# Kernel optimization log

Measured on AMD Instinct MI355X. Metric: run time of the kernel, lower is better.

Reference implementation:

```python
import jax, jax.numpy as jnp
import numpy as np

T_DIFF = 1000.0
LN_EPS = 1e-5


def _lin(x, w, b):
    return jnp.matmul(x, w.T) + b


def _ln(x, g, b):
    m = jnp.mean(x, axis=-1, keepdims=True)
    v = jnp.mean((x - m) ** 2, axis=-1, keepdims=True)
    return (x - m) / jnp.sqrt(v + LN_EPS) * g + b


def _pos_lin(x, w, b):
    return jnp.matmul(x, jax.nn.softplus(w).T) + b


def _gamma(t, g_l1_w, g_l1_b, g_l2_w, g_l2_b, g_l3_w, g_l3_b, gamma_0, gamma_1):
    def gtilde(u):
        l1 = _pos_lin(u, g_l1_w, g_l1_b)
        return l1 + _pos_lin(jax.nn.sigmoid(_pos_lin(l1, g_l2_w, g_l2_b)), g_l3_w, g_l3_b)
    g0, g1, gt = gtilde(jnp.zeros_like(t)), gtilde(jnp.ones_like(t)), gtilde(t)
    return gamma_0 + (gamma_1 - gamma_0) * (gt - g0) / (g1 - g0)


def _pair_dist(a):
    # safe pairwise euclidean distances, (B,N,N,1)
    diff = a[:, :, None, :] - a[:, None, :, :]
    d2 = jnp.sum(diff * diff, axis=-1, keepdims=True)
    return diff, jnp.sqrt(jnp.maximum(d2, 1e-12)), d2


def _egc_layer(x, h, x0, p):
    _, d0, _ = _pair_dist(x0)                      # original distances
    diff, dist, d2 = _pair_dist(x)                 # current distances (pre-LN x)
    h = _ln(h, p['lnh_g'], p['lnh_b'])
    x = _ln(x, p['lnx_g'], p['lnx_b'])
    B, N, F = h.shape
    h_i = jnp.broadcast_to(h[:, :, None, :], (B, N, N, F))
    h_j = jnp.broadcast_to(h[:, None, :, :], (B, N, N, F))
    einp = jnp.concatenate([h_i, h_j, d2, d0], axis=-1)  # (B,N,N,2F+2)
    m = jax.nn.silu(_lin(einp, p['edg1_w'], p['edg1_b']))
    m = jax.nn.silu(_lin(m, p['edg2_w'], p['edg2_b']))
    e = jax.nn.sigmoid(_lin(m, p['edgi_w'], p['edgi_b']))
    e = e * (1.0 - jnp.eye(N, dtype=e.dtype)[None, :, :, None])
    m_agg = jnp.sum(e * m, axis=2)                 # sum over j -> (B,N,F)
    hn = jax.nn.silu(_lin(jnp.concatenate([h, m_agg], axis=-1), p['node1_w'], p['node1_b']))
    hn = h + _lin(hn, p['node2_w'], p['node2_b'])
    cw = jax.nn.silu(_lin(einp, p['cor1_w'], p['cor1_b']))
    cw = jax.nn.silu(_lin(cw, p['cor2_w'], p['cor2_b']))
    cw = _lin(cw, p['cor3_w'], p['cor3_b'])        # (B,N,N,1)
    x_next = x + jnp.sum(cw * (diff / (dist + 1.0)), axis=2)
    return x_next, hn


def setup_inputs() -> dict:
    key = jax.random.key(0)
    ks = iter(jax.random.split(key, 64))
    B, N, H, L = 8, 192, 32, 4
    d = {}
    d['xyz_atom_species'] = jax.random.normal(next(ks), (B, N, 4), jnp.float32)
    d['pdf'] = jax.random.normal(next(ks), (B, 3000), jnp.float32)
    d['t'] = jax.random.uniform(next(ks), (B,), jnp.float32) * T_DIFF

    def w(k, shape):
        fan_in = shape[-1]
        return jax.random.normal(k, shape, jnp.float32) / np.sqrt(fan_in)

    d['emb_in_w'] = w(next(ks), (H, 12)); d['emb_in_b'] = jnp.zeros((H,), jnp.float32)
    d['emb_out_w'] = w(next(ks), (1, H)); d['emb_out_b'] = jnp.zeros((1,), jnp.float32)
    d['x_out_w'] = w(next(ks), (3, 3)); d['x_out_b'] = jnp.zeros((3,), jnp.float32)
    d['pdf_w'] = w(next(ks), (10, 3000)); d['pdf_b'] = jnp.zeros((10,), jnp.float32)
    d['g_l1_w'] = w(next(ks), (1, 1)); d['g_l1_b'] = jnp.zeros((1,), jnp.float32)
    d['g_l2_w'] = w(next(ks), (1024, 1)); d['g_l2_b'] = jnp.zeros((1024,), jnp.float32)
    d['g_l3_w'] = w(next(ks), (1, 1024)); d['g_l3_b'] = jnp.zeros((1,), jnp.float32)
    d['gamma_0'] = jnp.array([-5.0], jnp.float32)
    d['gamma_1'] = jnp.array([10.0], jnp.float32)
    d['lnh_g'] = jnp.ones((L, H), jnp.float32); d['lnh_b'] = jnp.zeros((L, H), jnp.float32)
    d['lnx_g'] = jnp.ones((L, 3), jnp.float32); d['lnx_b'] = jnp.zeros((L, 3), jnp.float32)
    d['edg1_w'] = w(next(ks), (L, H, 2 * H + 2)); d['edg1_b'] = jnp.zeros((L, H), jnp.float32)
    d['edg2_w'] = w(next(ks), (L, H, H)); d['edg2_b'] = jnp.zeros((L, H), jnp.float32)
    d['edgi_w'] = w(next(ks), (L, 1, H)); d['edgi_b'] = jnp.zeros((L, 1), jnp.float32)
    d['node1_w'] = w(next(ks), (L, H, 2 * H)); d['node1_b'] = jnp.zeros((L, H), jnp.float32)
    d['node2_w'] = w(next(ks), (L, H, H)); d['node2_b'] = jnp.zeros((L, H), jnp.float32)
    d['cor1_w'] = w(next(ks), (L, H, 2 * H + 2)); d['cor1_b'] = jnp.zeros((L, H), jnp.float32)
    d['cor2_w'] = w(next(ks), (L, H, H)); d['cor2_b'] = jnp.zeros((L, H), jnp.float32)
    d['cor3_w'] = w(next(ks), (L, 1, H)); d['cor3_b'] = jnp.zeros((L, 1), jnp.float32)
    return d


def reference(xyz_atom_species, pdf, t, emb_in_w, emb_in_b, emb_out_w, emb_out_b,
              x_out_w, x_out_b, pdf_w, pdf_b, g_l1_w, g_l1_b, g_l2_w, g_l2_b,
              g_l3_w, g_l3_b, gamma_0, gamma_1, lnh_g, lnh_b, lnx_g, lnx_b,
              edg1_w, edg1_b, edg2_w, edg2_b, edgi_w, edgi_b, node1_w, node1_b,
              node2_w, node2_b, cor1_w, cor1_b, cor2_w, cor2_b, cor3_w, cor3_b):
    B, N, _ = xyz_atom_species.shape
    h = xyz_atom_species[:, :, 3:4]                # (B,N,1)
    x = xyz_atom_species[:, :, :3]
    x0 = x
    tn = (t / T_DIFF)[:, None]                     # (B,1)
    t_emb = _gamma(tn, g_l1_w, g_l1_b, g_l2_w, g_l2_b, g_l3_w, g_l3_b, gamma_0, gamma_1)
    pdf_emb = _lin(pdf, pdf_w, pdf_b)              # (B,10)
    h = jnp.concatenate([
        h,
        jnp.broadcast_to(t_emb[:, None, :], (B, N, 1)),
        jnp.broadcast_to(pdf_emb[:, None, :], (B, N, 10)),
    ], axis=-1)
    h = _lin(h, emb_in_w, emb_in_b)                # (B,N,32)
    for l in range(4):
        p = dict(lnh_g=lnh_g[l], lnh_b=lnh_b[l], lnx_g=lnx_g[l], lnx_b=lnx_b[l],
                 edg1_w=edg1_w[l], edg1_b=edg1_b[l], edg2_w=edg2_w[l], edg2_b=edg2_b[l],
                 edgi_w=edgi_w[l], edgi_b=edgi_b[l], node1_w=node1_w[l], node1_b=node1_b[l],
                 node2_w=node2_w[l], node2_b=node2_b[l], cor1_w=cor1_w[l], cor1_b=cor1_b[l],
                 cor2_w=cor2_w[l], cor2_b=cor2_b[l], cor3_w=cor3_w[l], cor3_b=cor3_b[l])
        x, h = _egc_layer(x, h, x0, p)
    h = _lin(h, emb_out_w, emb_out_b)
    x = _lin(x, x_out_w, x_out_b) - x0
    return jnp.concatenate([x, h], axis=-1)        # (B,N,4)
```

## Files before the change

kernel.cpp:

```cpp
#include <hip/hip_runtime.h>
#include <hip/hip_bf16.h>
#include <math.h>

#define BATCH 8
#define NATOMS 192
#define HF 32

using short8 = __attribute__((ext_vector_type(8))) short;
using f32x4  = __attribute__((ext_vector_type(4))) float;

__device__ __forceinline__ float fast_rcp(float x){ return __builtin_amdgcn_rcpf(x); }
__device__ __forceinline__ float sigmoid_f(float x){ return fast_rcp(1.0f+__expf(-x)); }
__device__ __forceinline__ float silu_f(float x){ return x*fast_rcp(1.0f+__expf(-x)); }
__device__ __forceinline__ float softplus_f(float x){ return fmaxf(x,0.0f)+log1pf(expf(-fabsf(x))); }
__device__ __forceinline__ unsigned short f2bf(float x){
  __hip_bfloat16 h = __float2bfloat16(x);
  return __builtin_bit_cast(unsigned short, h);
}

__device__ __forceinline__ float wave_sum(float v){
  v += __shfl_xor(v, 1);
  v += __shfl_xor(v, 2);
  v += __shfl_xor(v, 4);
  v += __shfl_xor(v, 8);
  v += __shfl_xor(v, 16);
  v += __shfl_xor(v, 32);
  return v;
}

__global__ __launch_bounds__(256) void k_prelude(
    const float* __restrict__ pdf, const float* __restrict__ t,
    const float* __restrict__ pdf_w, const float* __restrict__ pdf_b,
    const float* __restrict__ g1w, const float* __restrict__ g1b,
    const float* __restrict__ g2w, const float* __restrict__ g2b,
    const float* __restrict__ g3w, const float* __restrict__ g3b,
    const float* __restrict__ gamma0, const float* __restrict__ gamma1,
    const float* __restrict__ e2w, const float* __restrict__ c2w,
    unsigned short* __restrict__ e2wb, unsigned short* __restrict__ c2wb,
    float* __restrict__ temb, float* __restrict__ pdfe)
{
  __shared__ float lds[4];
  const int bx = blockIdx.x, tid = threadIdx.x;
  const int wv = tid >> 6, ln = tid & 63;

  if (bx >= 88){
    const int g = (bx - 88)*256 + tid;
    e2wb[g] = f2bf(e2w[g]);
    c2wb[g] = f2bf(c2w[g]);
    return;
  }
  if (bx < 80){
    const int b = bx / 10, o = bx % 10;
    const float* pb = pdf + b*3000;
    const float* wb = pdf_w + o*3000;
    float p = 0.f;
    for (int k = tid; k < 3000; k += 256) p = fmaf(pb[k], wb[k], p);
    p = wave_sum(p);
    if (ln == 0) lds[wv] = p;
    __syncthreads();
    if (tid == 0) pdfe[b*10 + o] = lds[0] + lds[1] + lds[2] + lds[3] + pdf_b[o];
    return;
  }
  const int b = bx - 80;
  const float w1 = softplus_f(g1w[0]);
  const float b1 = g1b[0];
  const float tn = t[b] * (1.0f/1000.0f);
  const float l1_0 = b1;
  const float l1_1 = w1 + b1;
  const float l1_t = fmaf(w1, tn, b1);
  float a0 = 0.f, a1 = 0.f, at = 0.f;
  for (int k = tid; k < 1024; k += 256){
    float w2 = softplus_f(g2w[k]);
    float bb = g2b[k];
    float w3 = softplus_f(g3w[k]);
    a0 += sigmoid_f(fmaf(w2, l1_0, bb)) * w3;
    a1 += sigmoid_f(fmaf(w2, l1_1, bb)) * w3;
    at += sigmoid_f(fmaf(w2, l1_t, bb)) * w3;
  }
  float sums[3]; float vals[3] = {a0, a1, at};
  for (int r = 0; r < 3; ++r){
    float v = wave_sum(vals[r]);
    __syncthreads();
    if (ln == 0) lds[wv] = v;
    __syncthreads();
    sums[r] = lds[0] + lds[1] + lds[2] + lds[3];
  }
  if (tid == 0){
    const float b3 = g3b[0];
    const float g0 = l1_0 + sums[0] + b3;
    const float g1v = l1_1 + sums[1] + b3;
    const float gt = l1_t + sums[2] + b3;
    temb[b] = gamma0[0] + (gamma1[0] - gamma0[0]) * (gt - g0) / (g1v - g0);
  }
}

__global__ __launch_bounds__(256) void k_embed_node(
    const float* __restrict__ xyz, const float* __restrict__ temb,
    const float* __restrict__ pdfe, const float* __restrict__ wi,
    const float* __restrict__ bi,
    const float* __restrict__ lnhg, const float* __restrict__ lnhb,
    const float* __restrict__ e1w, const float* __restrict__ e1b,
    const float* __restrict__ c1w, const float* __restrict__ c1b,
    float* __restrict__ x, float* __restrict__ hln,
    float* __restrict__ ue, float* __restrict__ uc,
    float* __restrict__ vep, float* __restrict__ vcp)
{
  __shared__ float s_h[8][33];
  const int tid = threadIdx.x;
  const int il = tid >> 5, f = tid & 31;
  const int node = blockIdx.x*8 + il;
  const int b = node / NATOMS;

  {
    const float sp = xyz[node*4 + 3];
    const float* w = wi + f*12;
    float a = bi[f];
    a = fmaf(sp, w[0], a);
    a = fmaf(temb[b], w[1], a);
    const float* pe = pdfe + b*10;
#pragma unroll
    for (int p = 0; p < 10; ++p) a = fmaf(pe[p], w[2+p], a);
    s_h[il][f] = a;
  }
  if (f < 3) x[node*3 + f] = xyz[node*4 + f];
  __syncthreads();

  float hl[32];
  float m = 0.f;
#pragma unroll
  for (int k = 0; k < 32; ++k){ hl[k] = s_h[il][k]; m += hl[k]; }
  m *= (1.0f/32.0f);
  float v = 0.f;
#pragma unroll
  for (int k = 0; k < 32; ++k){ float d = hl[k]-m; v = fmaf(d, d, v); }
  float r = rsqrtf(v*(1.0f/32.0f) + 1e-5f);
#pragma unroll
  for (int k = 0; k < 32; ++k) hl[k] = fmaf((hl[k]-m)*r, lnhg[k], lnhb[k]);
  hln[node*32 + f] = hl[f];

  const float* we = e1w + f*66;
  float sv = e1b[f], su = 0.f;
#pragma unroll
  for (int k = 0; k < 32; ++k){ sv = fmaf(hl[k], we[k], sv); su = fmaf(hl[k], we[32+k], su); }
  vep[node*32 + f] = sv;
  ue [node*32 + f] = su;

  const float* wc = c1w + f*66;
  float cv = c1b[f], cu = 0.f;
#pragma unroll
  for (int k = 0; k < 32; ++k){ cv = fmaf(hl[k], wc[k], cv); cu = fmaf(hl[k], wc[32+k], cu); }
  vcp[node*32 + f] = cv;
  uc [node*32 + f] = cu;
}

__global__ __launch_bounds__(128, 3) void k_pair(
    const float* __restrict__ xin, const float* __restrict__ xyz,
    const float* __restrict__ hln, const float* __restrict__ ue,
    const float* __restrict__ uc, const float* __restrict__ vep,
    const float* __restrict__ vcp,
    const float* __restrict__ e1w, const float* __restrict__ c1w,
    const unsigned short* __restrict__ e2wb, const unsigned short* __restrict__ c2wb,
    const float* __restrict__ e2b, const float* __restrict__ eiw,
    const float* __restrict__ eib,
    const float* __restrict__ c2b, const float* __restrict__ c3w,
    const float* __restrict__ c3b,
    const float* __restrict__ n1w, const float* __restrict__ n1b,
    const float* __restrict__ n2w, const float* __restrict__ n2b,
    const float* __restrict__ lnxg, const float* __restrict__ lnxb,
    const float* __restrict__ lnhg_n, const float* __restrict__ lnhb_n,
    const float* __restrict__ e1w_n, const float* __restrict__ e1b_n,
    const float* __restrict__ c1w_n, const float* __restrict__ c1b_n,
    float* __restrict__ hln_n, float* __restrict__ ue_n,
    float* __restrict__ uc_n, float* __restrict__ vep_n,
    float* __restrict__ vcp_n, float* __restrict__ xout,
    const float* __restrict__ how, const float* __restrict__ hob,
    const float* __restrict__ xow, const float* __restrict__ xob,
    float* __restrict__ dout, const int lastl)
{
  __shared__ float s_geo[64][6];
  __shared__ unsigned short s_m1[64][40];
  __shared__ unsigned short s_c1[64][40];
  __shared__ unsigned short s_we[32][40];
  __shared__ unsigned short s_wc[32][40];
  __shared__ float s_xc[3];

  const int i = blockIdx.x, b = blockIdx.y;
  const int tid = threadIdx.x;
  const int base = b * NATOMS;
  const int node = base + i;
  const int lane = tid & 63;
  const int n = lane & 15, quad = lane >> 4;

  {
    const short8* es = (const short8*)e2wb;
    const short8* cs = (const short8*)c2wb;
    const int f = tid >> 2, kq = tid & 3;
    *(short8*)&s_we[f][kq*8] = es[tid];
    *(short8*)&s_wc[f][kq*8] = cs[tid];
  }

  const int kk = tid & 31, jg = tid >> 5;
  const float vpe = vep[node*32 + kk];
  const float vpc = vcp[node*32 + kk];
  const float we64 = e1w[kk*66 + 64], we65 = e1w[kk*66 + 65];
  const float wc64 = c1w[kk*66 + 64], wc65 = c1w[kk*66 + 65];

  const float eb0 = e2b[n], eb1 = e2b[16 + n];
  const float ew0 = eiw[n], ew1 = eiw[16 + n];
  const float ebias = eib[0];
  const float cb0 = c2b[n], cb1 = c2b[16 + n];
  const float cw0 = c3w[n], cw1 = c3w[16 + n];
  const float cbias = c3b[0];

  float ma0 = 0.f, ma1 = 0.f;
  float px = 0.f, py = 0.f, pz = 0.f;

  for (int chunk = 0; chunk < 3; ++chunk){
    if (tid < 64){
      const int jj = tid;
      const int j = chunk*64 + jj;
      const float* xi_p = xin + node*3;
      const float* xj_p = xin + (base + j)*3;
      const float dfx = xi_p[0] - xj_p[0], dfy = xi_p[1] - xj_p[1], dfz = xi_p[2] - xj_p[2];
      const float d2 = dfx*dfx + dfy*dfy + dfz*dfz;
      const float dist = sqrtf(fmaxf(d2, 1e-12f));
      const float* x0i = xyz + node*4;
      const float* x0j = xyz + (base + j)*4;
      const float q0 = x0i[0]-x0j[0], q1 = x0i[1]-x0j[1], q2 = x0i[2]-x0j[2];
      const float d0 = sqrtf(fmaxf(q0*q0 + q1*q1 + q2*q2, 1e-12f));
      s_geo[jj][0] = dfx; s_geo[jj][1] = dfy; s_geo[jj][2] = dfz;
      s_geo[jj][3] = d2;  s_geo[jj][4] = d0;  s_geo[jj][5] = dist;
    }
    __syncthreads();

#pragma unroll
    for (int jj = jg; jj < 64; jj += 4){
      const float d2 = s_geo[jj][3], d0 = s_geo[jj][4];
      const int j = chunk*64 + jj;
      const float uev = ue[(size_t)(base + j)*32 + kk];
      const float m1 = silu_f(fmaf(d2, we64, fmaf(d0, we65, vpe + uev)));
      s_m1[jj][kk] = f2bf(m1);
      const float ucv = uc[(size_t)(base + j)*32 + kk];
      const float c1 = silu_f(fmaf(d2, wc64, fmaf(d0, wc65, vpc + ucv)));
      s_c1[jj][kk] = f2bf(c1);
    }
    __syncthreads();

    if (tid < 64){
      short8 b0 = *(const short8*)&s_we[n][quad*8];
      short8 b1 = *(const short8*)&s_we[16 + n][quad*8];
#pragma unroll
      for (int jt = 0; jt < 4; ++jt){
        short8 a = *(const short8*)&s_m1[jt*16 + n][quad*8];
        f32x4 z = {0.f, 0.f, 0.f, 0.f};
        f32x4 acc0 = __builtin_amdgcn_mfma_f32_16x16x32_bf16(a, b0, z, 0, 0, 0);
        f32x4 acc1 = __builtin_amdgcn_mfma_f32_16x16x32_bf16(a, b1, z, 0, 0, 0);
        float m20[4], m21[4], g[4];
#pragma unroll
        for (int r = 0; r < 4; ++r){
          m20[r] = silu_f(acc0[r] + eb0);
          m21[r] = silu_f(acc1[r] + eb1);
          g[r] = m20[r]*ew0 + m21[r]*ew1;
        }
#pragma unroll
        for (int r = 0; r < 4; ++r){
          g[r] += __shfl_xor(g[r], 1);
          g[r] += __shfl_xor(g[r], 2);
          g[r] += __shfl_xor(g[r], 4);
          g[r] += __shfl_xor(g[r], 8);
        }
#pragma unroll
        for (int r = 0; r < 4; ++r){
          const int jglob = chunk*64 + jt*16 + quad*4 + r;
          const float e = (jglob == i) ? 0.0f : sigmoid_f(g[r] + ebias);
          ma0 = fmaf(e, m20[r], ma0);
          ma1 = fmaf(e, m21[r], ma1);
        }
      }
    } else {
      short8 b0 = *(const short8*)&s_wc[n][quad*8];
      short8 b1 = *(const short8*)&s_wc[16 + n][quad*8];
#pragma unroll
      for (int jt = 0; jt < 4; ++jt){
        short8 a = *(const short8*)&s_c1[jt*16 + n][quad*8];
        f32x4 z = {0.f, 0.f, 0.f, 0.f};
        f32x4 acc0 = __builtin_amdgcn_mfma_f32_16x16x32_bf16(a, b0, z, 0, 0, 0);
        f32x4 acc1 = __builtin_amdgcn_mfma_f32_16x16x32_bf16(a, b1, z, 0, 0, 0);
        float g[4];
#pragma unroll
        for (int r = 0; r < 4; ++r){
          g[r] = silu_f(acc0[r] + cb0)*cw0 + silu_f(acc1[r] + cb1)*cw1;
        }
#pragma unroll
        for (int r = 0; r < 4; ++r){
          g[r] += __shfl_xor(g[r], 1);
          g[r] += __shfl_xor(g[r], 2);
          g[r] += __shfl_xor(g[r], 4);
          g[r] += __shfl_xor(g[r], 8);
        }
#pragma unroll
        for (int r = 0; r < 4; ++r){
          const int jj = jt*16 + quad*4 + r;
          const float s = (g[r] + cbias) * fast_rcp(s_geo[jj][5] + 1.0f);
          px = fmaf(s, s_geo[jj][0], px);
          py = fmaf(s, s_geo[jj][1], py);
          pz = fmaf(s, s_geo[jj][2], pz);
        }
      }
    }
    __syncthreads();
  }

  if (tid < 64){
    ma0 += __shfl_xor(ma0, 16); ma0 += __shfl_xor(ma0, 32);
    ma1 += __shfl_xor(ma1, 16); ma1 += __shfl_xor(ma1, 32);
  } else {
    px += __shfl_xor(px, 16); px += __shfl_xor(px, 32);
    py += __shfl_xor(py, 16); py += __shfl_xor(py, 32);
    pz += __shfl_xor(pz, 16); pz += __shfl_xor(pz, 32);
    if (lane == 0){ s_xc[0] = px; s_xc[1] = py; s_xc[2] = pz; }
  }
  __syncthreads();
  if (tid >= 64) return;

  const int f = tid & 31;
  const float mgf = (tid & 16) ? ma1 : ma0;
  const float hlf = hln[node*32 + f];

  float a = n1b[f];
  const float* w1 = n1w + f*64;
#pragma unroll
  for (int k = 0; k < 32; ++k) a = fmaf(__shfl(hlf, k, 64), w1[k], a);
#pragma unroll
  for (int k = 0; k < 32; ++k) a = fmaf(__shfl(mgf, k, 64), w1[32 + k], a);
  const float n1v = silu_f(a);
  float o = n2b[f];
  const float* w2 = n2w + f*32;
#pragma unroll
  for (int k = 0; k < 32; ++k) o = fmaf(__shfl(n1v, k, 64), w2[k], o);
  const float ho = hlf + o;

  float xn0, xn1, xn2;
  {
    const float* xr = xin + node*3;
    const float x0 = xr[0], x1 = xr[1], x2 = xr[2];
    const float mx = (x0 + x1 + x2) * (1.0f/3.0f);
    const float v0 = x0-mx, v1 = x1-mx, v2 = x2-mx;
    const float r = rsqrtf((v0*v0 + v1*v1 + v2*v2)*(1.0f/3.0f) + 1e-5f);
    xn0 = fmaf(v0*r, lnxg[0], lnxb[0]) + s_xc[0];
    xn1 = fmaf(v1*r, lnxg[1], lnxb[1]) + s_xc[1];
    xn2 = fmaf(v2*r, lnxg[2], lnxb[2]) + s_xc[2];
  }

  if (!lastl){
    if (tid == 0){
      float* xo = xout + node*3;
      xo[0] = xn0; xo[1] = xn1; xo[2] = xn2;
    }
    float s = ho;
    s += __shfl_xor(s, 1); s += __shfl_xor(s, 2); s += __shfl_xor(s, 4);
    s += __shfl_xor(s, 8); s += __shfl_xor(s, 16);
    const float m = s * (1.0f/32.0f);
    const float d = ho - m;
    float vv = d*d;
    vv += __shfl_xor(vv, 1); vv += __shfl_xor(vv, 2); vv += __shfl_xor(vv, 4);
    vv += __shfl_xor(vv, 8); vv += __shfl_xor(vv, 16);
    const float r = rsqrtf(vv*(1.0f/32.0f) + 1e-5f);
    const float hl = fmaf(d*r, lnhg_n[f], lnhb_n[f]);
    if (tid < 32) hln_n[node*32 + f] = hl;

    const float* we = e1w_n + f*66;
    const float* wc = c1w_n + f*66;
    float sv = e1b_n[f], su = 0.f, cv = c1b_n[f], cu = 0.f;
#pragma unroll
    for (int k = 0; k < 32; ++k){
      const float tkk = __shfl(hl, k, 64);
      sv = fmaf(tkk, we[k], sv);
      su = fmaf(tkk, we[32 + k], su);
      cv = fmaf(tkk, wc[k], cv);
      cu = fmaf(tkk, wc[32 + k], cu);
    }
    if (tid < 32){
      vep_n[node*32 + f] = sv;
      ue_n [node*32 + f] = su;
      vcp_n[node*32 + f] = cv;
      uc_n [node*32 + f] = cu;
    }
  } else {
    float hh = how[f] * ho;
    hh += __shfl_xor(hh, 1); hh += __shfl_xor(hh, 2); hh += __shfl_xor(hh, 4);
    hh += __shfl_xor(hh, 8); hh += __shfl_xor(hh, 16);
    if (tid == 0) dout[node*4 + 3] = hh + hob[0];
    if (tid < 3){
      const int c = tid;
      float oo = xob[c];
      oo = fmaf(xn0, xow[c*3 + 0], oo);
      oo = fmaf(xn1, xow[c*3 + 1], oo);
      oo = fmaf(xn2, xow[c*3 + 2], oo);
      dout[node*4 + c] = oo - xyz[node*4 + c];
    }
  }
}

extern "C" void kernel_launch(void* const* d_in, const int* in_sizes, int n_in,
                              void* d_out, int out_size, void* d_ws, size_t ws_size,
                              hipStream_t stream)
{
  const float* xyz      = (const float*)d_in[0];
  const float* pdf      = (const float*)d_in[1];
  const float* t        = (const float*)d_in[2];
  const float* emb_in_w = (const float*)d_in[3];
  const float* emb_in_b = (const float*)d_in[4];
  const float* emb_out_w= (const float*)d_in[5];
  const float* emb_out_b= (const float*)d_in[6];
  const float* x_out_w  = (const float*)d_in[7];
  const float* x_out_b  = (const float*)d_in[8];
  const float* pdf_w    = (const float*)d_in[9];
  const float* pdf_b    = (const float*)d_in[10];
  const float* g1w      = (const float*)d_in[11];
  const float* g1b      = (const float*)d_in[12];
  const float* g2w      = (const float*)d_in[13];
  const float* g2b      = (const float*)d_in[14];
  const float* g3w      = (const float*)d_in[15];
  const float* g3b      = (const float*)d_in[16];
  const float* gamma0   = (const float*)d_in[17];
  const float* gamma1   = (const float*)d_in[18];
  const float* lnhg     = (const float*)d_in[19];
  const float* lnhb     = (const float*)d_in[20];
  const float* lnxg     = (const float*)d_in[21];
  const float* lnxb     = (const float*)d_in[22];
  const float* e1w      = (const float*)d_in[23];
  const float* e1b      = (const float*)d_in[24];
  const float* e2w      = (const float*)d_in[25];
  const float* e2b      = (const float*)d_in[26];
  const float* eiw      = (const float*)d_in[27];
  const float* eib      = (const float*)d_in[28];
  const float* n1w      = (const float*)d_in[29];
  const float* n1b      = (const float*)d_in[30];
  const float* n2w      = (const float*)d_in[31];
  const float* n2b      = (const float*)d_in[32];
  const float* c1w      = (const float*)d_in[33];
  const float* c1b      = (const float*)d_in[34];
  const float* c2w      = (const float*)d_in[35];
  const float* c2b      = (const float*)d_in[36];
  const float* c3w      = (const float*)d_in[37];
  const float* c3b      = (const float*)d_in[38];

  const int NTOT = BATCH*NATOMS;
  float* ws   = (float*)d_ws;
  float* temb = ws;
  float* pdfe = ws + 8;
  unsigned short* e2wb = (unsigned short*)(ws + 96);
  unsigned short* c2wb = e2wb + 4096;
  float* p0   = ws + 96 + 4096;
  float* xbA  = p0;                float* xbB  = xbA + NTOT*3;
  float* hlnA = xbB  + NTOT*3;     float* hlnB = hlnA + NTOT*32;
  float* ueA  = hlnB + NTOT*32;    float* ueB  = ueA  + NTOT*32;
  float* ucA  = ueB  + NTOT*32;    float* ucB  = ucA  + NTOT*32;
  float* vepA = ucB  + NTOT*32;    float* vepB = vepA + NTOT*32;
  float* vcpA = vepB + NTOT*32;    float* vcpB = vcpA + NTOT*32;

  float* xb[2]  = {xbA,  xbB};
  float* hlnP[2]= {hlnA, hlnB};
  float* ueP[2] = {ueA,  ueB};
  float* ucP[2] = {ucA,  ucB};
  float* vepP[2]= {vepA, vepB};
  float* vcpP[2]= {vcpA, vcpB};

  k_prelude<<<104, 256, 0, stream>>>(pdf, t, pdf_w, pdf_b,
      g1w, g1b, g2w, g2b, g3w, g3b, gamma0, gamma1,
      e2w, c2w, e2wb, c2wb, temb, pdfe);
  k_embed_node<<<NTOT/8, 256, 0, stream>>>(
      xyz, temb, pdfe, emb_in_w, emb_in_b,
      lnhg, lnhb, e1w, e1b, c1w, c1b,
      xbA, hlnA, ueA, ucA, vepA, vcpA);

  for (int l = 0; l < 4; ++l){
    const int p = l & 1;
    const int nl = (l < 3) ? (l + 1) : 3;
    k_pair<<<dim3(NATOMS, BATCH), 128, 0, stream>>>(
        xb[p], xyz, hlnP[p], ueP[p], ucP[p], vepP[p], vcpP[p],
        e1w + l*2112, c1w + l*2112,
        e2wb + l*1024, c2wb + l*1024,
        e2b + l*32, eiw + l*32, eib + l,
        c2b + l*32, c3w + l*32, c3b + l,
        n1w + l*2048, n1b + l*32, n2w + l*1024, n2b + l*32,
        lnxg + l*3, lnxb + l*3,
        lnhg + nl*32, lnhb + nl*32,
        e1w + nl*2112, e1b + nl*32, c1w + nl*2112, c1b + nl*32,
        hlnP[1-p], ueP[1-p], ucP[1-p], vepP[1-p], vcpP[1-p], xb[1-p],
        emb_out_w, emb_out_b, x_out_w, x_out_b,
        (float*)d_out, (l == 3) ? 1 : 0);
  }
}
```

Measured before the change: 286.6 us.

## Process all three j-chunks in parallel with 384-thread blocks

The pair kernel now uses 384 threads per block: three 128-thread groups each handle one 64-atom chunk at the same time, instead of looping over the chunks with syncthreads between them. Per-group partial message and coordinate sums go through shared memory and are combined at the end. This removes the serial chunk loop and most barriers and exposes more waves per block. In exchange it uses more shared memory per block, and the node MLP tail still runs on only 64 threads while the other waves idle.

```diff
diff --git a/kernel.cpp b/kernel.cpp
--- a/kernel.cpp
+++ b/kernel.cpp
@@ -153,7 +153,7 @@
   uc [node*32 + f] = cu;
 }
 
-__global__ __launch_bounds__(128, 3) void k_pair(
+__global__ __launch_bounds__(384, 2) void k_pair(
     const float* __restrict__ xin, const float* __restrict__ xyz,
     const float* __restrict__ hln, const float* __restrict__ ue,
     const float* __restrict__ uc, const float* __restrict__ vep,
@@ -177,154 +177,158 @@
     const float* __restrict__ xow, const float* __restrict__ xob,
     float* __restrict__ dout, const int lastl)
 {
-  __shared__ float s_geo[64][6];
-  __shared__ unsigned short s_m1[64][40];
-  __shared__ unsigned short s_c1[64][40];
+  __shared__ float s_geo[NATOMS][6];
+  __shared__ unsigned short s_m1[NATOMS][40];
+  __shared__ unsigned short s_c1[NATOMS][40];
   __shared__ unsigned short s_we[32][40];
   __shared__ unsigned short s_wc[32][40];
-  __shared__ float s_xc[3];
+  __shared__ float s_pm[3][32];
+  __shared__ float s_pxc[3][3];
 
   const int i = blockIdx.x, b = blockIdx.y;
   const int tid = threadIdx.x;
   const int base = b * NATOMS;
   const int node = base + i;
-  const int lane = tid & 63;
+  const int g = tid >> 7;
+  const int t = tid & 127;
+  const int lane = t & 63;
+  const int isCor = t >> 6;
   const int n = lane & 15, quad = lane >> 4;
 
-  {
+  if (tid < NATOMS){
+    const int j = tid;
+    const float* xi_p = xin + node*3;
+    const float* xj_p = xin + (base + j)*3;
+    const float dfx = xi_p[0] - xj_p[0], dfy = xi_p[1] - xj_p[1], dfz = xi_p[2] - xj_p[2];
+    const float d2 = dfx*dfx + dfy*dfy + dfz*dfz;
+    const float dist = sqrtf(fmaxf(d2, 1e-12f));
+    const float* x0i = xyz + node*4;
+    const float* x0j = xyz + (base + j)*4;
+    const float q0 = x0i[0]-x0j[0], q1 = x0i[1]-x0j[1], q2 = x0i[2]-x0j[2];
+    const float d0 = sqrtf(fmaxf(q0*q0 + q1*q1 + q2*q2, 1e-12f));
+    s_geo[j][0] = dfx; s_geo[j][1] = dfy; s_geo[j][2] = dfz;
+    s_geo[j][3] = d2;  s_geo[j][4] = d0;  s_geo[j][5] = dist;
+  } else {
+    const int u = tid - NATOMS;
     const short8* es = (const short8*)e2wb;
     const short8* cs = (const short8*)c2wb;
-    const int f = tid >> 2, kq = tid & 3;
-    *(short8*)&s_we[f][kq*8] = es[tid];
-    *(short8*)&s_wc[f][kq*8] = cs[tid];
-  }
-
-  const int kk = tid & 31, jg = tid >> 5;
-  const float vpe = vep[node*32 + kk];
-  const float vpc = vcp[node*32 + kk];
-  const float we64 = e1w[kk*66 + 64], we65 = e1w[kk*66 + 65];
-  const float wc64 = c1w[kk*66 + 64], wc65 = c1w[kk*66 + 65];
-
-  const float eb0 = e2b[n], eb1 = e2b[16 + n];
-  const float ew0 = eiw[n], ew1 = eiw[16 + n];
-  const float ebias = eib[0];
-  const float cb0 = c2b[n], cb1 = c2b[16 + n];
-  const float cw0 = c3w[n], cw1 = c3w[16 + n];
-  const float cbias = c3b[0];
-
-  float ma0 = 0.f, ma1 = 0.f;
-  float px = 0.f, py = 0.f, pz = 0.f;
-
-  for (int chunk = 0; chunk < 3; ++chunk){
-    if (tid < 64){
-      const int jj = tid;
-      const int j = chunk*64 + jj;
-      const float* xi_p = xin + node*3;
-      const float* xj_p = xin + (base + j)*3;
-      const float dfx = xi_p[0] - xj_p[0], dfy = xi_p[1] - xj_p[1], dfz = xi_p[2] - xj_p[2];
-      const float d2 = dfx*dfx + dfy*dfy + dfz*dfz;
-      const float dist = sqrtf(fmaxf(d2, 1e-12f));
-      const float* x0i = xyz + node*4;
-      const float* x0j = xyz + (base + j)*4;
-      const float q0 = x0i[0]-x0j[0], q1 = x0i[1]-x0j[1], q2 = x0i[2]-x0j[2];
-      const float d0 = sqrtf(fmaxf(q0*q0 + q1*q1 + q2*q2, 1e-12f));
-      s_geo[jj][0] = dfx; s_geo[jj][1] = dfy; s_geo[jj][2] = dfz;
-      s_geo[jj][3] = d2;  s_geo[jj][4] = d0;  s_geo[jj][5] = dist;
-    }
-    __syncthreads();
-
+    if (u < 128){
+      const int f = u >> 2, kq = u & 3;
+      *(short8*)&s_we[f][kq*8] = es[u];
+    }
+    if (u >= 64){
+      const int c = u - 64;
+      const int f = c >> 2, kq = c & 3;
+      *(short8*)&s_wc[f][kq*8] = cs[c];
+    }
+  }
+  __syncthreads();
+
+  {
+    const int kk = t & 31, jg = t >> 5;
+    const float vpe = vep[node*32 + kk];
+    const float vpc = vcp[node*32 + kk];
+    const float we64 = e1w[kk*66 + 64], we65 = e1w[kk*66 + 65];
+    const float wc64 = c1w[kk*66 + 64], wc65 = c1w[kk*66 + 65];
 #pragma unroll
     for (int jj = jg; jj < 64; jj += 4){
-      const float d2 = s_geo[jj][3], d0 = s_geo[jj][4];
-      const int j = chunk*64 + jj;
-      const float uev = ue[(size_t)(base + j)*32 + kk];
+      const int row = g*64 + jj;
+      const float d2 = s_geo[row][3], d0 = s_geo[row][4];
+      const float uev = ue[(size_t)(base + row)*32 + kk];
       const float m1 = silu_f(fmaf(d2, we64, fmaf(d0, we65, vpe + uev)));
-      s_m1[jj][kk] = f2bf(m1);
-      const float ucv = uc[(size_t)(base + j)*32 + kk];
+      s_m1[row][kk] = f2bf(m1);
+      const float ucv = uc[(size_t)(base + row)*32 + kk];
       const float c1 = silu_f(fmaf(d2, wc64, fmaf(d0, wc65, vpc + ucv)));
-      s_c1[jj][kk] = f2bf(c1);
-    }
-    __syncthreads();
-
-    if (tid < 64){
-      short8 b0 = *(const short8*)&s_we[n][quad*8];
-      short8 b1 = *(const short8*)&s_we[16 + n][quad*8];
-#pragma unroll
-      for (int jt = 0; jt < 4; ++jt){
-        short8 a = *(const short8*)&s_m1[jt*16 + n][quad*8];
-        f32x4 z = {0.f, 0.f, 0.f, 0.f};
-        f32x4 acc0 = __builtin_amdgcn_mfma_f32_16x16x32_bf16(a, b0, z, 0, 0, 0);
-        f32x4 acc1 = __builtin_amdgcn_mfma_f32_16x16x32_bf16(a, b1, z, 0, 0, 0);
-        float m20[4], m21[4], g[4];
-#pragma unroll
-        for (int r = 0; r < 4; ++r){
-          m20[r] = silu_f(acc0[r] + eb0);
-          m21[r] = silu_f(acc1[r] + eb1);
-          g[r] = m20[r]*ew0 + m21[r]*ew1;
-        }
-#pragma unroll
-        for (int r = 0; r < 4; ++r){
-          g[r] += __shfl_xor(g[r], 1);
-          g[r] += __shfl_xor(g[r], 2);
-          g[r] += __shfl_xor(g[r], 4);
-          g[r] += __shfl_xor(g[r], 8);
-        }
-#pragma unroll
-        for (int r = 0; r < 4; ++r){
-          const int jglob = chunk*64 + jt*16 + quad*4 + r;
-          const float e = (jglob == i) ? 0.0f : sigmoid_f(g[r] + ebias);
-          ma0 = fmaf(e, m20[r], ma0);
-          ma1 = fmaf(e, m21[r], ma1);
-        }
-      }
-    } else {
-      short8 b0 = *(const short8*)&s_wc[n][quad*8];
-      short8 b1 = *(const short8*)&s_wc[16 + n][quad*8];
-#pragma unroll
-      for (int jt = 0; jt < 4; ++jt){
-        short8 a = *(const short8*)&s_c1[jt*16 + n][quad*8];
-        f32x4 z = {0.f, 0.f, 0.f, 0.f};
-        f32x4 acc0 = __builtin_amdgcn_mfma_f32_16x16x32_bf16(a, b0, z, 0, 0, 0);
-        f32x4 acc1 = __builtin_amdgcn_mfma_f32_16x16x32_bf16(a, b1, z, 0, 0, 0);
-        float g[4];
-#pragma unroll
-        for (int r = 0; r < 4; ++r){
-          g[r] = silu_f(acc0[r] + cb0)*cw0 + silu_f(acc1[r] + cb1)*cw1;
-        }
-#pragma unroll
-        for (int r = 0; r < 4; ++r){
-          g[r] += __shfl_xor(g[r], 1);
-          g[r] += __shfl_xor(g[r], 2);
-          g[r] += __shfl_xor(g[r], 4);
-          g[r] += __shfl_xor(g[r], 8);
-        }
-#pragma unroll
-        for (int r = 0; r < 4; ++r){
-          const int jj = jt*16 + quad*4 + r;
-          const float s = (g[r] + cbias) * fast_rcp(s_geo[jj][5] + 1.0f);
-          px = fmaf(s, s_geo[jj][0], px);
-          py = fmaf(s, s_geo[jj][1], py);
-          pz = fmaf(s, s_geo[jj][2], pz);
-        }
-      }
-    }
-    __syncthreads();
-  }
-
-  if (tid < 64){
+      s_c1[row][kk] = f2bf(c1);
+    }
+  }
+  __syncthreads();
+
+  if (isCor == 0){
+    const float eb0 = e2b[n], eb1 = e2b[16 + n];
+    const float ew0 = eiw[n], ew1 = eiw[16 + n];
+    const float ebias = eib[0];
+    float ma0 = 0.f, ma1 = 0.f;
+    short8 b0 = *(const short8*)&s_we[n][quad*8];
+    short8 b1 = *(const short8*)&s_we[16 + n][quad*8];
+#pragma unroll
+    for (int jt = 0; jt < 4; ++jt){
+      short8 a = *(const short8*)&s_m1[g*64 + jt*16 + n][quad*8];
+      f32x4 z = {0.f, 0.f, 0.f, 0.f};
+      f32x4 acc0 = __builtin_amdgcn_mfma_f32_16x16x32_bf16(a, b0, z, 0, 0, 0);
+      f32x4 acc1 = __builtin_amdgcn_mfma_f32_16x16x32_bf16(a, b1, z, 0, 0, 0);
+      float m20[4], m21[4], gg[4];
+#pragma unroll
+      for (int r = 0; r < 4; ++r){
+        m20[r] = silu_f(acc0[r] + eb0);
+        m21[r] = silu_f(acc1[r] + eb1);
+        gg[r] = m20[r]*ew0 + m21[r]*ew1;
+      }
+#pragma unroll
+      for (int r = 0; r < 4; ++r){
+        gg[r] += __shfl_xor(gg[r], 1);
+        gg[r] += __shfl_xor(gg[r], 2);
+        gg[r] += __shfl_xor(gg[r], 4);
+        gg[r] += __shfl_xor(gg[r], 8);
+      }
+#pragma unroll
+      for (int r = 0; r < 4; ++r){
+        const int jglob = g*64 + jt*16 + quad*4 + r;
+        const float e = (jglob == i) ? 0.0f : sigmoid_f(gg[r] + ebias);
+        ma0 = fmaf(e, m20[r], ma0);
+        ma1 = fmaf(e, m21[r], ma1);
+      }
+    }
     ma0 += __shfl_xor(ma0, 16); ma0 += __shfl_xor(ma0, 32);
     ma1 += __shfl_xor(ma1, 16); ma1 += __shfl_xor(ma1, 32);
+    if (lane < 16){
+      s_pm[g][lane] = ma0;
+      s_pm[g][16 + lane] = ma1;
+    }
   } else {
+    const float cb0 = c2b[n], cb1 = c2b[16 + n];
+    const float cw0 = c3w[n], cw1 = c3w[16 + n];
+    const float cbias = c3b[0];
+    float px = 0.f, py = 0.f, pz = 0.f;
+    short8 b0 = *(const short8*)&s_wc[n][quad*8];
+    short8 b1 = *(const short8*)&s_wc[16 + n][quad*8];
+#pragma unroll
+    for (int jt = 0; jt < 4; ++jt){
+      short8 a = *(const short8*)&s_c1[g*64 + jt*16 + n][quad*8];
+      f32x4 z = {0.f, 0.f, 0.f, 0.f};
+      f32x4 acc0 = __builtin_amdgcn_mfma_f32_16x16x32_bf16(a, b0, z, 0, 0, 0);
+      f32x4 acc1 = __builtin_amdgcn_mfma_f32_16x16x32_bf16(a, b1, z, 0, 0, 0);
+      float gg[4];
+#pragma unroll
+      for (int r = 0; r < 4; ++r){
+        gg[r] = silu_f(acc0[r] + cb0)*cw0 + silu_f(acc1[r] + cb1)*cw1;
+      }
+#pragma unroll
+      for (int r = 0; r < 4; ++r){
+        gg[r] += __shfl_xor(gg[r], 1);
+        gg[r] += __shfl_xor(gg[r], 2);
+        gg[r] += __shfl_xor(gg[r], 4);
+        gg[r] += __shfl_xor(gg[r], 8);
+      }
+#pragma unroll
+      for (int r = 0; r < 4; ++r){
+        const int row = g*64 + jt*16 + quad*4 + r;
+        const float s = (gg[r] + cbias) * fast_rcp(s_geo[row][5] + 1.0f);
+        px = fmaf(s, s_geo[row][0], px);
+        py = fmaf(s, s_geo[row][1], py);
+        pz = fmaf(s, s_geo[row][2], pz);
+      }
+    }
     px += __shfl_xor(px, 16); px += __shfl_xor(px, 32);
     py += __shfl_xor(py, 16); py += __shfl_xor(py, 32);
     pz += __shfl_xor(pz, 16); pz += __shfl_xor(pz, 32);
-    if (lane == 0){ s_xc[0] = px; s_xc[1] = py; s_xc[2] = pz; }
+    if (lane == 0){ s_pxc[g][0] = px; s_pxc[g][1] = py; s_pxc[g][2] = pz; }
   }
   __syncthreads();
   if (tid >= 64) return;
 
   const int f = tid & 31;
-  const float mgf = (tid & 16) ? ma1 : ma0;
+  const float mgf = s_pm[0][f] + s_pm[1][f] + s_pm[2][f];
   const float hlf = hln[node*32 + f];
 
   float a = n1b[f];
@@ -347,9 +351,9 @@
     const float mx = (x0 + x1 + x2) * (1.0f/3.0f);
     const float v0 = x0-mx, v1 = x1-mx, v2 = x2-mx;
     const float r = rsqrtf((v0*v0 + v1*v1 + v2*v2)*(1.0f/3.0f) + 1e-5f);
-    xn0 = fmaf(v0*r, lnxg[0], lnxb[0]) + s_xc[0];
-    xn1 = fmaf(v1*r, lnxg[1], lnxb[1]) + s_xc[1];
-    xn2 = fmaf(v2*r, lnxg[2], lnxb[2]) + s_xc[2];
+    xn0 = fmaf(v0*r, lnxg[0], lnxb[0]) + s_pxc[0][0] + s_pxc[1][0] + s_pxc[2][0];
+    xn1 = fmaf(v1*r, lnxg[1], lnxb[1]) + s_pxc[0][1] + s_pxc[1][1] + s_pxc[2][1];
+    xn2 = fmaf(v2*r, lnxg[2], lnxb[2]) + s_pxc[0][2] + s_pxc[1][2] + s_pxc[2][2];
   }
 
   if (!lastl){
@@ -478,7 +482,7 @@
   for (int l = 0; l < 4; ++l){
     const int p = l & 1;
     const int nl = (l < 3) ? (l + 1) : 3;
-    k_pair<<<dim3(NATOMS, BATCH), 128, 0, stream>>>(
+    k_pair<<<dim3(NATOMS, BATCH), 384, 0, stream>>>(
         xb[p], xyz, hlnP[p], ueP[p], ucP[p], vepP[p], vcpP[p],
         e1w + l*2112, c1w + l*2112,
         e2wb + l*1024, c2wb + l*1024,
```

After: 275.4 us. 1.04x faster.
